# Performance work log

Measured on AMD Instinct MI355X. Metric: run time of the kernel, lower is better.

The kernel has to match this reference:

```python
import jax, jax.numpy as jnp
import numpy as np

D_MODEL, HQ, HKV = 2048, 32, 8
DK = D_MODEL // HQ          # 64
GROUP = HQ // HKV           # 4 query heads per kv head
B, S = 1, 2048


def setup_inputs() -> dict:
    key = jax.random.key(0)
    ks = jax.random.split(key, 5)
    sc = 0.02
    return {
        "x":  jax.random.normal(ks[0], (B, S, D_MODEL), jnp.float32),
        "wq": jax.random.normal(ks[1], (D_MODEL, D_MODEL), jnp.float32) * sc,
        "bq": jnp.zeros((D_MODEL,), jnp.float32),
        "wk": jax.random.normal(ks[2], (HKV * DK, D_MODEL), jnp.float32) * sc,
        "bk": jnp.zeros((HKV * DK,), jnp.float32),
        "wv": jax.random.normal(ks[3], (HKV * DK, D_MODEL), jnp.float32) * sc,
        "bv": jnp.zeros((HKV * DK,), jnp.float32),
        "wo": jax.random.normal(ks[4], (D_MODEL, D_MODEL), jnp.float32) * sc,
        "bo": jnp.zeros((D_MODEL,), jnp.float32),
    }


def reference(x, wq, bq, wk, bk, wv, bv, wo, bo):
    b, s, _ = x.shape
    scale = 1.0 / jnp.sqrt(jnp.asarray(DK, x.dtype))
    # projections (torch Linear: y = x @ W.T + b)
    q = (x @ wq.T + bq).reshape(b, s, HKV, GROUP, DK)   # [B,S,Hkv,G,Dk]
    k = (x @ wk.T + bk).reshape(b, s, HKV, DK)          # [B,S,Hkv,Dk]
    v = (x @ wv.T + bv).reshape(b, s, HKV, DK)
    # GQA: broadcast each kv head over its GROUP query heads (no repeat_interleave)
    scores = jnp.einsum("bshgd,bthd->bhgst", q, k) * scale   # [B,Hkv,G,S,S]
    causal = jnp.tril(jnp.ones((s, s), bool))
    scores = jnp.where(causal, scores, jnp.asarray(-jnp.inf, scores.dtype))
    attn = jax.nn.softmax(scores, axis=-1)
    out = jnp.einsum("bhgst,bthd->bshgd", attn, v)           # [B,S,Hkv,G,Dk]
    out = out.reshape(b, s, D_MODEL)
    return out @ wo.T + bo
```

## Files before the change

### kernel.cpp

```cpp
#include <hip/hip_runtime.h>


#define S_LEN 2048
#define DM    2048
#define QKVW  3072

typedef float  f32x4  __attribute__((ext_vector_type(4)));
typedef float  f32x16 __attribute__((ext_vector_type(16)));
typedef __bf16 bf16x8 __attribute__((ext_vector_type(8)));
typedef unsigned short u16;
typedef unsigned int   u32;
typedef u16 u16x8 __attribute__((ext_vector_type(8)));
typedef u32 u32x4 __attribute__((ext_vector_type(4)));

__device__ __forceinline__ u16 f2b(float f) {
    __bf16 h = (__bf16)f;
    return __builtin_bit_cast(unsigned short, h);
}
__device__ __forceinline__ u32 pk2(float lo, float hi) {
    return (u32)f2b(lo) | ((u32)f2b(hi) << 16);
}

#define MFMA16(a, b, c) __builtin_amdgcn_mfma_f32_16x16x32_bf16((a), (b), (c), 0, 0, 0)
#define MFMA32(a, b, c) __builtin_amdgcn_mfma_f32_32x32x16_bf16((a), (b), (c), 0, 0, 0)

__device__ __forceinline__ void gld16(const void* g, void* l) {
    __builtin_amdgcn_global_load_lds(
        (const __attribute__((address_space(1))) void*)g,
        (__attribute__((address_space(3))) void*)l, 16, 0, 0);
}

__global__ __launch_bounds__(256) void cvt5(
    const float* __restrict__ x,  const float* __restrict__ wq,
    const float* __restrict__ wk, const float* __restrict__ wv,
    const float* __restrict__ wo,
    const float* __restrict__ bq, const float* __restrict__ bk,
    const float* __restrict__ bv,
    u16* __restrict__ xb, u16* __restrict__ wqkvb, u16* __restrict__ wob,
    float* __restrict__ bqkv)
{
    if (blockIdx.x == 7168) {
        for (int i = threadIdx.x; i < 3072; i += 256)
            bqkv[i] = (i < 2048) ? bq[i] : (i < 2560 ? bk[i - 2048] : bv[i - 2560]);
        return;
    }
    int i = blockIdx.x * 256 + threadIdx.x;
    const float* s; u16* d; int off;
    if      (i < 524288)  { s = x;  d = xb;    off = i; }
    else if (i < 1048576) { s = wq; d = wqkvb; off = i - 524288; }
    else if (i < 1179648) { s = wk; d = wqkvb + (size_t)2048 * 2048; off = i - 1048576; }
    else if (i < 1310720) { s = wv; d = wqkvb + (size_t)2560 * 2048; off = i - 1179648; }
    else                  { s = wo; d = wob;   off = i - 1310720; }
    const float4* s4 = (const float4*)s;
    float4 a = s4[2 * (size_t)off], b = s4[2 * (size_t)off + 1];
    u16x8 o;
    o[0] = f2b(a.x); o[1] = f2b(a.y); o[2] = f2b(a.z); o[3] = f2b(a.w);
    o[4] = f2b(b.x); o[5] = f2b(b.y); o[6] = f2b(b.z); o[7] = f2b(b.w);
    ((u16x8*)d)[(size_t)off] = o;
}

template <bool OUT_BF16, bool QSCALE>
__global__ __launch_bounds__(256) void gemm_nt64(
    const u16* __restrict__ A, const u16* __restrict__ B,
    const float* __restrict__ bias, void* __restrict__ Cv,
    int N, int K, int nxb)
{
    __shared__ u16 As[128 * 32];
    __shared__ u16 Bs[64 * 32];
    const int nwg = gridDim.x;
    const int bid = blockIdx.x;
    const int wg  = (bid & 7) * (nwg >> 3) + (bid >> 3);
    const int bm  = (wg / nxb) * 128;
    const int bn  = (wg % nxb) * 64;

    const int tid  = threadIdx.x;
    const int lane = tid & 63;
    const int w    = tid >> 6;
    const int wr   = w >> 1, wc = w & 1;
    const int la = lane & 15, lg = lane >> 4;
    const int srow = lane >> 2;
    const int sseg = (lane & 3) * 8;

    f32x4 acc[4][2] = {};

    for (int k0 = 0; k0 < K; k0 += 32) {
        #pragma unroll
        for (int i = 0; i < 2; ++i) {
            const int c = w * 2 + i;
            gld16(A + (size_t)(bm + c * 16 + srow) * K + k0 + sseg, As + c * 512);
        }
        gld16(B + (size_t)(bn + w * 16 + srow) * K + k0 + sseg, Bs + w * 512);
        __syncthreads();
        bf16x8 af[4], bf[2];
        #pragma unroll
        for (int m = 0; m < 4; ++m)
            af[m] = *(const bf16x8*)(As + (wr * 64 + m * 16 + la) * 32 + lg * 8);
        #pragma unroll
        for (int n = 0; n < 2; ++n)
            bf[n] = *(const bf16x8*)(Bs + (wc * 32 + n * 16 + la) * 32 + lg * 8);
        #pragma unroll
        for (int m = 0; m < 4; ++m)
            #pragma unroll
            for (int n = 0; n < 2; ++n)
                acc[m][n] = MFMA16(af[m], bf[n], acc[m][n]);
        __syncthreads();
    }

    #pragma unroll
    for (int m = 0; m < 4; ++m) {
        #pragma unroll
        for (int n = 0; n < 2; ++n) {
            const int col = bn + wc * 32 + n * 16 + la;
            const float bb = bias[col];
            const float osc = (QSCALE && col < 2048) ? 0.180336881f : 1.0f;
            #pragma unroll
            for (int j = 0; j < 4; ++j) {
                const int row = bm + wr * 64 + m * 16 + lg * 4 + j;
                const float v = (acc[m][n][j] + bb) * osc;
                if (OUT_BF16) ((u16*)Cv)[(size_t)row * N + col] = f2b(v);
                else          ((float*)Cv)[(size_t)row * N + col] = v;
            }
        }
    }
}

__global__ __launch_bounds__(256) void kvrepack(const u16* __restrict__ QKVb,
                                                u16* __restrict__ Kp,
                                                u16* __restrict__ Vt) {
    const int h   = blockIdx.y;
    const int kt  = blockIdx.x;
    const int tid = threadIdx.x;
    __shared__ u16 T[64][72];
    #pragma unroll
    for (int p = 0; p < 2; ++p) {
        const int idx = p * 256 + tid;
        const int r   = idx >> 3;
        const int c8  = (idx & 7) * 8;
        *(u16x8*)&Kp[((size_t)h * S_LEN + kt * 64 + r) * 64 + c8] =
            *(const u16x8*)&QKVb[(size_t)(kt * 64 + r) * QKVW + 2048 + h * 64 + c8];
    }
    #pragma unroll
    for (int p = 0; p < 2; ++p) {
        const int r  = p * 32 + (tid >> 3);
        const int cs = (tid & 7) * 8;
        u16x8 v = *(const u16x8*)&QKVb[(size_t)(kt * 64 + r) * QKVW + 2560 + h * 64 + cs];
        #pragma unroll
        for (int j = 0; j < 8; ++j) T[r][cs + j] = v[j];
    }
    __syncthreads();
    #pragma unroll
    for (int p = 0; p < 2; ++p) {
        const int d  = p * 32 + (tid >> 3);
        const int ks = (tid & 7) * 8;
        u16x8 o;
        #pragma unroll
        for (int j = 0; j < 8; ++j) o[j] = T[ks + j][d];
        *(u16x8*)&Vt[((size_t)h * 64 + d) * S_LEN + kt * 64 + ks] = o;
    }
}

__global__ __launch_bounds__(512, 4) void attn(
    const u16* __restrict__ Qb,
    const u16* __restrict__ Kp,
    const u16* __restrict__ Vt,
    u16* __restrict__ Ob)
{
    const int tid  = threadIdx.x;
    const int lane = tid & 63;
    const int w    = tid >> 6;
    const int head = w & 3;
    const int par  = w >> 2;
    const int bid  = blockIdx.x;
    const int band = (bid < 256) ? (63 - (bid >> 3)) : ((bid - 256) >> 3);
    const int h    = bid & 7;
    const int hq   = h * 4 + head;
    const int q0   = band * 32;
    const int lq   = lane & 31;
    const int hi   = lane >> 5;

    __shared__ char LDS[65536];

    bf16x8 qf[4];
    #pragma unroll
    for (int ds = 0; ds < 4; ++ds)
        qf[ds] = *(const bf16x8*)&Qb[(size_t)(q0 + lq) * QKVW + hq * 64 + ds * 16 + hi * 8];

    f32x16 ot[2] = {};
    float m = -3e38f, lsum = 0.f;

    const char* Khb = (const char*)(Kp + (size_t)h * S_LEN * 64);
    const char* Vhb = (const char*)(Vt + (size_t)h * 64 * S_LEN);

    const int r0 = tid >> 3;
    const int s0 = (((tid & 7) ^ (r0 & 7)) << 4);
    const int woff = w * 1024;

    const int nch = (band >> 1) + 1;
    const int nit = (nch + 1) >> 1;

    auto stage_pair = [&](int j) {
        const int pb = (j & 1) * 16384;
        const size_t kr = (size_t)(j * 128 + r0);
        gld16(Khb + (kr << 7) + s0,          LDS + pb + woff);
        gld16(Khb + ((kr + 64) << 7) + s0,   LDS + pb + 8192 + woff);
        const size_t vb = ((size_t)r0 << 12) + (size_t)(j * 256) + s0;
        gld16(Vhb + vb,        LDS + 32768 + pb + woff);
        gld16(Vhb + vb + 128,  LDS + 32768 + pb + 8192 + woff);
    };

    stage_pair(0);
    __syncthreads();

    for (int i = 0; i < nit; ++i) {
        if (i + 1 < nit) stage_pair(i + 1);

        const int cg = 2 * i + par;
        if (cg < nch) {
            const int base = (i & 1) * 16384 + par * 8192;
            const char* Kb = LDS + base;
            const char* Vb = LDS + 32768 + base;
            const int k0 = cg * 64;

            f32x16 s[2];
            __builtin_amdgcn_s_setprio(1);
            #pragma unroll
            for (int kt = 0; kt < 2; ++kt) {
                f32x16 acc = {};
                #pragma unroll
                for (int ds = 0; ds < 4; ++ds) {
                    const int key = kt * 32 + lq;
                    const int byteK = (key << 7) + ((ds * 32 + hi * 16) ^ ((key & 7) << 4));
                    bf16x8 kf = *(const bf16x8*)(Kb + byteK);
                    acc = MFMA32(kf, qf[ds], acc);
                }
                s[kt] = acc;
            }
            __builtin_amdgcn_s_setprio(0);

            if (k0 + 63 > q0) {
                #pragma unroll
                for (int kt = 0; kt < 2; ++kt)
                    #pragma unroll
                    for (int r = 0; r < 16; ++r) {
                        const int key = k0 + kt * 32 + (r & 3) + 8 * (r >> 2) + 4 * hi;
                        if (key > q0 + lq) s[kt][r] = -1e30f;
                    }
            }

            float a16[16];
            #pragma unroll
            for (int r = 0; r < 16; ++r) a16[r] = fmaxf(s[0][r], s[1][r]);
            #pragma unroll
            for (int r = 0; r < 8; ++r) a16[r] = fmaxf(a16[r], a16[r + 8]);
            #pragma unroll
            for (int r = 0; r < 4; ++r) a16[r] = fmaxf(a16[r], a16[r + 4]);
            float pm = fmaxf(fmaxf(a16[0], a16[1]), fmaxf(a16[2], a16[3]));
            pm = fmaxf(pm, __shfl_xor(pm, 32));

            if (!__all(pm <= m + 11.5f)) {
                const float mn   = fmaxf(m, pm);
                const float corr = __builtin_exp2f(m - mn);
                m = mn;
                lsum *= corr;
                #pragma unroll
                for (int r = 0; r < 16; ++r) {
                    const int row = (r & 3) + 8 * (r >> 2) + 4 * hi;
                    const float cr = __shfl(corr, row);
                    ot[0][r] *= cr;
                    ot[1][r] *= cr;
                }
            }

            float ps = 0.f;
            #pragma unroll
            for (int kt = 0; kt < 2; ++kt)
                #pragma unroll
                for (int r = 0; r < 16; ++r) {
                    const float p = __builtin_exp2f(s[kt][r] - m);
                    s[kt][r] = p;
                    ps += p;
                }
            lsum += ps + __shfl_xor(ps, 32);

            bf16x8 pa[4];
            #pragma unroll
            for (int kb = 0; kb < 4; ++kb) {
                const int kt = kb >> 1;
                const int rb = (kb & 1) * 8;
                const u32 A = pk2(s[kt][rb + 0], s[kt][rb + 1]);
                const u32 B = pk2(s[kt][rb + 4], s[kt][rb + 5]);
                const u32 C = pk2(s[kt][rb + 2], s[kt][rb + 3]);
                const u32 D = pk2(s[kt][rb + 6], s[kt][rb + 7]);
                const u32 sA = __shfl_xor(A, 32), sB = __shfl_xor(B, 32);
                const u32 sC = __shfl_xor(C, 32), sD = __shfl_xor(D, 32);
                u32x4 t4;
                t4[0] = hi ? sB : A;
                t4[1] = hi ? sD : C;
                t4[2] = hi ? B : sA;
                t4[3] = hi ? D : sC;
                pa[kb] = __builtin_bit_cast(bf16x8, t4);
            }

            __builtin_amdgcn_s_setprio(1);
            #pragma unroll
            for (int dt = 0; dt < 2; ++dt)
                #pragma unroll
                for (int kb = 0; kb < 4; ++kb) {
                    const int d = dt * 32 + lq;
                    const int byteV = (d << 7) + ((kb * 32 + hi * 16) ^ ((d & 7) << 4));
                    bf16x8 vf = *(const bf16x8*)(Vb + byteV);
                    ot[dt] = MFMA32(pa[kb], vf, ot[dt]);
                }
            __builtin_amdgcn_s_setprio(0);
        }

        __syncthreads();
    }

    float* Uls = (float*)LDS;
    float* Mls = (float*)(LDS + 32768);
    float* Lls = (float*)(LDS + 33280);

    if (par == 1) {
        #pragma unroll
        for (int r = 0; r < 16; ++r) {
            const int row = (r & 3) + 8 * (r >> 2) + 4 * hi;
            Uls[(head * 32 + row) * 64 + lq]      = ot[0][r];
            Uls[(head * 32 + row) * 64 + 32 + lq] = ot[1][r];
        }
        if (lane < 32) { Mls[head * 32 + lane] = m; Lls[head * 32 + lane] = lsum; }
    }
    __syncthreads();
    if (par == 1) return;

    const float m1  = Mls[head * 32 + lq];
    const float l1  = Lls[head * 32 + lq];
    const float M   = fmaxf(m, m1);
    const float a0  = __builtin_exp2f(m - M);
    const float a1  = __builtin_exp2f(m1 - M);
    const float inv = 1.f / (a0 * lsum + a1 * l1);

    #pragma unroll
    for (int r = 0; r < 16; ++r) {
        const int row = (r & 3) + 8 * (r >> 2) + 4 * hi;
        const float a0r = __shfl(a0, row);
        const float a1r = __shfl(a1, row);
        const float ivr = __shfl(inv, row);
        #pragma unroll
        for (int dt = 0; dt < 2; ++dt) {
            const float u1 = Uls[(head * 32 + row) * 64 + dt * 32 + lq];
            Ob[(size_t)(q0 + row) * DM + hq * 64 + dt * 32 + lq] =
                f2b((a0r * ot[dt][r] + a1r * u1) * ivr);
        }
    }
}

extern "C" void kernel_launch(void* const* d_in, const int* in_sizes, int n_in,
                              void* d_out, int out_size, void* d_ws, size_t ws_size,
                              hipStream_t stream)
{
    const float* x  = (const float*)d_in[0];
    const float* wq = (const float*)d_in[1];
    const float* bq = (const float*)d_in[2];
    const float* wk = (const float*)d_in[3];
    const float* bk = (const float*)d_in[4];
    const float* wv = (const float*)d_in[5];
    const float* bv = (const float*)d_in[6];
    const float* wo = (const float*)d_in[7];
    const float* bo = (const float*)d_in[8];
    float* out = (float*)d_out;

    char* ws = (char*)d_ws;
    u16* xb     = (u16*)(ws);
    u16* wqkvb  = (u16*)(ws + (8u  << 20));
    u16* wob    = (u16*)(ws + (20u << 20));
    u16* QKVb   = (u16*)(ws + (28u << 20));
    float* bqkv = (float*)(ws + (40u << 20));
    u16* Ob = xb;
    u16* Kp = wqkvb;
    u16* Vt = wqkvb + (size_t)2 * 1024 * 1024 / 2;

    cvt5<<<7169, 256, 0, stream>>>(x, wq, wk, wv, wo, bq, bk, bv,
                                   xb, wqkvb, wob, bqkv);
    gemm_nt64<true, true><<<768, 256, 0, stream>>>(
        xb, wqkvb, bqkv, QKVb, QKVW, 2048, QKVW / 64);
    kvrepack<<<dim3(32, 8), 256, 0, stream>>>(QKVb, Kp, Vt);
    attn<<<512, 512, 0, stream>>>(QKVb, Kp, Vt, Ob);
    gemm_nt64<false, false><<<512, 256, 0, stream>>>(
        Ob, wob, bo, out, DM, 2048, DM / 64);
}
```

Measured before the change: 149.2 us.

## Widen GEMM K-step to 64 and use max3 tree in softmax row max

The projection GEMM now loads a 64-wide K slice per iteration, split into two 32-wide LDS halves, and runs two MFMA sub-steps between barriers. This halves the number of __syncthreads and loop iterations per tile, in exchange for double the LDS footprint. The attention row-max reduction is rewritten as a tree of three-input max operations so the compiler can emit v_max3, cutting ALU instruction count. The arrays are named as two buffers but are not used for load/compute overlap.

```diff
diff --git a/kernel.cpp b/kernel.cpp
--- a/kernel.cpp
+++ b/kernel.cpp
@@ -19,6 +19,9 @@
 }
 __device__ __forceinline__ u32 pk2(float lo, float hi) {
     return (u32)f2b(lo) | ((u32)f2b(hi) << 16);
+}
+__device__ __forceinline__ float max3f(float a, float b, float c) {
+    return fmaxf(fmaxf(a, b), c);
 }
 
 #define MFMA16(a, b, c) __builtin_amdgcn_mfma_f32_16x16x32_bf16((a), (b), (c), 0, 0, 0)
@@ -65,8 +68,8 @@
     const float* __restrict__ bias, void* __restrict__ Cv,
     int N, int K, int nxb)
 {
-    __shared__ u16 As[128 * 32];
-    __shared__ u16 Bs[64 * 32];
+    __shared__ u16 As[2][128 * 32];
+    __shared__ u16 Bs[2][64 * 32];
     const int nwg = gridDim.x;
     const int bid = blockIdx.x;
     const int wg  = (bid & 7) * (nwg >> 3) + (bid >> 3);
@@ -78,31 +81,49 @@
     const int w    = tid >> 6;
     const int wr   = w >> 1, wc = w & 1;
     const int la = lane & 15, lg = lane >> 4;
-    const int srow = lane >> 2;
-    const int sseg = (lane & 3) * 8;
 
     f32x4 acc[4][2] = {};
 
-    for (int k0 = 0; k0 < K; k0 += 32) {
+    char* const abase = (char*)&As[0][0] + w * 1024;
+    char* const bbase = (char*)&Bs[0][0] + w * 1024;
+
+    for (int k0 = 0; k0 < K; k0 += 64) {
+        #pragma unroll
+        for (int i = 0; i < 4; ++i) {
+            const int c   = tid + 256 * i;
+            const int kh  = c >> 9;
+            const int rem = c & 511;
+            const int row = rem >> 2;
+            const int seg = rem & 3;
+            gld16(A + (size_t)(bm + row) * K + k0 + kh * 32 + seg * 8,
+                  abase + i * 4096);
+        }
         #pragma unroll
         for (int i = 0; i < 2; ++i) {
-            const int c = w * 2 + i;
-            gld16(A + (size_t)(bm + c * 16 + srow) * K + k0 + sseg, As + c * 512);
-        }
-        gld16(B + (size_t)(bn + w * 16 + srow) * K + k0 + sseg, Bs + w * 512);
+            const int c   = tid + 256 * i;
+            const int kh  = c >> 8;
+            const int rem = c & 255;
+            const int row = rem >> 2;
+            const int seg = rem & 3;
+            gld16(B + (size_t)(bn + row) * K + k0 + kh * 32 + seg * 8,
+                  bbase + i * 4096);
+        }
         __syncthreads();
-        bf16x8 af[4], bf[2];
-        #pragma unroll
-        for (int m = 0; m < 4; ++m)
-            af[m] = *(const bf16x8*)(As + (wr * 64 + m * 16 + la) * 32 + lg * 8);
-        #pragma unroll
-        for (int n = 0; n < 2; ++n)
-            bf[n] = *(const bf16x8*)(Bs + (wc * 32 + n * 16 + la) * 32 + lg * 8);
-        #pragma unroll
-        for (int m = 0; m < 4; ++m)
+        #pragma unroll
+        for (int kh = 0; kh < 2; ++kh) {
+            bf16x8 af[4], bf[2];
+            #pragma unroll
+            for (int m = 0; m < 4; ++m)
+                af[m] = *(const bf16x8*)(&As[kh][0] + (wr * 64 + m * 16 + la) * 32 + lg * 8);
             #pragma unroll
             for (int n = 0; n < 2; ++n)
-                acc[m][n] = MFMA16(af[m], bf[n], acc[m][n]);
+                bf[n] = *(const bf16x8*)(&Bs[kh][0] + (wc * 32 + n * 16 + la) * 32 + lg * 8);
+            #pragma unroll
+            for (int m = 0; m < 4; ++m)
+                #pragma unroll
+                for (int n = 0; n < 2; ++n)
+                    acc[m][n] = MFMA16(af[m], bf[n], acc[m][n]);
+        }
         __syncthreads();
     }
 
@@ -247,14 +268,18 @@
                     }
             }
 
-            float a16[16];
-            #pragma unroll
-            for (int r = 0; r < 16; ++r) a16[r] = fmaxf(s[0][r], s[1][r]);
-            #pragma unroll
-            for (int r = 0; r < 8; ++r) a16[r] = fmaxf(a16[r], a16[r + 8]);
-            #pragma unroll
-            for (int r = 0; r < 4; ++r) a16[r] = fmaxf(a16[r], a16[r + 4]);
-            float pm = fmaxf(fmaxf(a16[0], a16[1]), fmaxf(a16[2], a16[3]));
+            float t10[11];
+            #pragma unroll
+            for (int r = 0; r < 10; ++r)
+                t10[r] = max3f(s[(3*r) >> 4][(3*r) & 15],
+                               s[(3*r+1) >> 4][(3*r+1) & 15],
+                               s[(3*r+2) >> 4][(3*r+2) & 15]);
+            t10[10] = fmaxf(s[1][14], s[1][15]);
+            const float x0 = max3f(t10[0], t10[1], t10[2]);
+            const float x1 = max3f(t10[3], t10[4], t10[5]);
+            const float x2 = max3f(t10[6], t10[7], t10[8]);
+            const float x3 = fmaxf(t10[9], t10[10]);
+            float pm = fmaxf(max3f(x0, x1, x2), x3);
             pm = fmaxf(pm, __shfl_xor(pm, 32));
 
             if (!__all(pm <= m + 11.5f)) {
```

Result: faster. 137.6 us (-7.8%).
